# Optimization experiments

Hardware: AMD Instinct MI355X
Metric: run time of the kernel (lower is better)

Reference implementation:

```python
import jax, jax.numpy as jnp
import numpy as np

B, N, M = 4, 8192, 8192


def setup_inputs() -> dict:
    key = jax.random.key(0)
    k1, k2, k3, k4 = jax.random.split(key, 4)
    xyz1 = jax.random.normal(k1, (B, N, 3), dtype=jnp.float32)
    xyz2 = jax.random.normal(k2, (B, M, 3), dtype=jnp.float32)
    weights1 = jax.random.uniform(k3, (B, N), dtype=jnp.float32)
    weights2 = jax.random.uniform(k4, (B, M), dtype=jnp.float32)
    return {"xyz1": xyz1, "xyz2": xyz2, "weights1": weights1, "weights2": weights2}


def _chamfer_dists(xyz1, xyz2):
    # Squared L2 pairwise distances via the ||a||^2 + ||b||^2 - 2 a.b identity
    # (avoids materializing a [B, N, M, 3] difference tensor).
    sq1 = jnp.sum(xyz1 * xyz1, axis=-1)            # [B, N]
    sq2 = jnp.sum(xyz2 * xyz2, axis=-1)            # [B, M]
    dots = jnp.einsum("bnc,bmc->bnm", xyz1, xyz2)  # [B, N, M]
    d = sq1[:, :, None] + sq2[:, None, :] - 2.0 * dots
    d = jnp.maximum(d, 0.0)
    dist1 = jnp.min(d, axis=2)  # [B, N] nearest in xyz2 for each point in xyz1
    dist2 = jnp.min(d, axis=1)  # [B, M] nearest in xyz1 for each point in xyz2
    return dist1, dist2


def reference(xyz1, xyz2, weights1, weights2):
    dist1, dist2 = _chamfer_dists(xyz1, xyz2)
    dist1 = dist1 * weights1
    dist2 = dist2 * weights2
    dist1_avg = jnp.sum(dist1) / jnp.sum(weights1)
    dist2_avg = jnp.sum(dist2) / jnp.sum(weights2)
    return (dist1_avg + dist2_avg) / 2.0
```

## Files before the change

kernel.cpp:

```cpp
#include <hip/hip_runtime.h>

#define TPB 256
constexpr int Bsz  = 4;
constexpr int Npts = 8192;
constexpr int Mpts = 8192;
constexpr int PTS  = Bsz * Npts;
constexpr int Q    = 8;
constexpr int QPB  = TPB * Q;
constexpr int S    = 64;
constexpr int CPS  = Mpts / S;
constexpr int RBLK = 64;

__global__ void __launch_bounds__(TPB, 4) chamfer_min_kernel(
    const float* __restrict__ xyz1, const float* __restrict__ xyz2,
    unsigned int* __restrict__ partials)
{
    const int chunksPerDir = PTS / QPB;
    const int half = chunksPerDir * S;
    int bid = blockIdx.x;
    int dir = (bid >= half) ? 1 : 0;
    int id  = bid - dir * half;
    int s     = id % S;
    int chunk = id / S;
    int batch = chunk / (Npts / QPB);
    int qbase = chunk * QPB + threadIdx.x;

    const float* qsrc = dir ? xyz2 : xyz1;
    const float* csrc = dir ? xyz1 : xyz2;

    __shared__ float4 scand[CPS];
    int c0i = batch * Mpts + s * CPS;
    if (threadIdx.x < CPS) {
        int ci = c0i + threadIdx.x;
        float x = csrc[ci * 3 + 0];
        float y = csrc[ci * 3 + 1];
        float z = csrc[ci * 3 + 2];
        scand[threadIdx.x] =
            make_float4(-2.f * x, -2.f * y, -2.f * z, x * x + y * y + z * z);
    }

    float qx[Q], qy[Q], qz[Q], best[Q];
#pragma unroll
    for (int k = 0; k < Q; ++k) {
        int q = qbase + k * TPB;
        qx[k] = qsrc[q * 3 + 0];
        qy[k] = qsrc[q * 3 + 1];
        qz[k] = qsrc[q * 3 + 2];
        best[k] = 3.4e38f;
    }
    __syncthreads();

#pragma unroll 2
    for (int j = 0; j < CPS; j += 4) {
        float4 c0 = scand[j + 0];
        float4 c1 = scand[j + 1];
        float4 c2 = scand[j + 2];
        float4 c3 = scand[j + 3];
#pragma unroll
        for (int k = 0; k < Q; ++k) {
            float t0 = fmaf(qx[k], c0.x, fmaf(qy[k], c0.y, fmaf(qz[k], c0.z, c0.w)));
            float t1 = fmaf(qx[k], c1.x, fmaf(qy[k], c1.y, fmaf(qz[k], c1.z, c1.w)));
            float t2 = fmaf(qx[k], c2.x, fmaf(qy[k], c2.y, fmaf(qz[k], c2.z, c2.w)));
            float t3 = fmaf(qx[k], c3.x, fmaf(qy[k], c3.y, fmaf(qz[k], c3.z, c3.w)));
            best[k] = fminf(fminf(best[k], t0), t1);
            best[k] = fminf(fminf(best[k], t2), t3);
        }
    }

    unsigned int* pbase = partials + dir * PTS;
#pragma unroll
    for (int k = 0; k < Q; ++k) {
        int q = qbase + k * TPB;
        float sq = fmaf(qx[k], qx[k], fmaf(qy[k], qy[k], qz[k] * qz[k]));
        float d  = fmaxf(best[k] + sq, 0.f);
        atomicMin(&pbase[q], __float_as_uint(d));
    }
}

__global__ void __launch_bounds__(TPB) reduce_kernel(
    const float* __restrict__ partials,
    const float* __restrict__ w1, const float* __restrict__ w2,
    float2* __restrict__ slots)
{
    int gid = blockIdx.x * TPB + threadIdx.x;
    int dir = gid >> 13;
    int idx = gid & 8191;
    const float4* d4 = (const float4*)(partials + (size_t)dir * PTS);
    const float4* w4 = (const float4*)(dir ? w2 : w1);
    float4 d = d4[idx], w = w4[idx];
    float c = d.x * w.x + d.y * w.y + d.z * w.z + d.w * w.w;
    float s = w.x + w.y + w.z + w.w;

    for (int off = 32; off; off >>= 1) {
        c += __shfl_down(c, off);
        s += __shfl_down(s, off);
    }
    __shared__ float sc[4], ss[4];
    int lane = threadIdx.x & 63, wid = threadIdx.x >> 6;
    if (lane == 0) { sc[wid] = c; ss[wid] = s; }
    __syncthreads();
    if (threadIdx.x == 0) {
        slots[blockIdx.x] =
            make_float2(sc[0] + sc[1] + sc[2] + sc[3],
                        ss[0] + ss[1] + ss[2] + ss[3]);
    }
}

__global__ void __launch_bounds__(64) final_kernel(
    const float2* __restrict__ slots, float* __restrict__ out)
{
    float2 v = slots[threadIdx.x];
    for (int off = 16; off; off >>= 1) {
        v.x += __shfl_down(v.x, off, 32);
        v.y += __shfl_down(v.y, off, 32);
    }
    float c1 = __shfl(v.x, 32), s1 = __shfl(v.y, 32);
    if (threadIdx.x == 0)
        out[0] = 0.5f * (v.x / v.y + c1 / s1);
}

extern "C" void kernel_launch(void* const* d_in, const int* in_sizes, int n_in,
                              void* d_out, int out_size, void* d_ws, size_t ws_size,
                              hipStream_t stream) {
    const float* xyz1 = (const float*)d_in[0];
    const float* xyz2 = (const float*)d_in[1];
    const float* w1   = (const float*)d_in[2];
    const float* w2   = (const float*)d_in[3];
    float* out = (float*)d_out;

    unsigned int* partials = (unsigned int*)d_ws;
    float2* slots = (float2*)((char*)d_ws + (size_t)2 * PTS * sizeof(unsigned int));

    int half = (PTS / QPB) * S;
    chamfer_min_kernel<<<2 * half, TPB, 0, stream>>>(xyz1, xyz2, partials);
    reduce_kernel<<<RBLK, TPB, 0, stream>>>((const float*)partials, w1, w2, slots);
    final_kernel<<<1, 64, 0, stream>>>(slots, out);
}
```

Before: 101.0 us.

## Double queries per thread, halve candidate splits, replace atomicMin with per-split partials

```diff
diff --git a/kernel.cpp b/kernel.cpp
--- a/kernel.cpp
+++ b/kernel.cpp
@@ -5,15 +5,15 @@
 constexpr int Npts = 8192;
 constexpr int Mpts = 8192;
 constexpr int PTS  = Bsz * Npts;
-constexpr int Q    = 8;
+constexpr int Q    = 16;
 constexpr int QPB  = TPB * Q;
-constexpr int S    = 64;
+constexpr int S    = 32;
 constexpr int CPS  = Mpts / S;
 constexpr int RBLK = 64;
 
-__global__ void __launch_bounds__(TPB, 4) chamfer_min_kernel(
+__global__ void __launch_bounds__(TPB, 2) chamfer_min_kernel(
     const float* __restrict__ xyz1, const float* __restrict__ xyz2,
-    unsigned int* __restrict__ partials)
+    float* __restrict__ partials)
 {
     const int chunksPerDir = PTS / QPB;
     const int half = chunksPerDir * S;
@@ -29,9 +29,8 @@
     const float* csrc = dir ? xyz1 : xyz2;
 
     __shared__ float4 scand[CPS];
-    int c0i = batch * Mpts + s * CPS;
-    if (threadIdx.x < CPS) {
-        int ci = c0i + threadIdx.x;
+    {
+        int ci = batch * Mpts + s * CPS + threadIdx.x;
         float x = csrc[ci * 3 + 0];
         float y = csrc[ci * 3 + 1];
         float z = csrc[ci * 3 + 2];
@@ -67,13 +66,12 @@
         }
     }
 
-    unsigned int* pbase = partials + dir * PTS;
+    float* pbase = partials + (size_t)s * (2 * PTS) + (size_t)dir * PTS;
 #pragma unroll
     for (int k = 0; k < Q; ++k) {
         int q = qbase + k * TPB;
         float sq = fmaf(qx[k], qx[k], fmaf(qy[k], qy[k], qz[k] * qz[k]));
-        float d  = fmaxf(best[k] + sq, 0.f);
-        atomicMin(&pbase[q], __float_as_uint(d));
+        pbase[q] = fmaxf(best[k] + sq, 0.f);
     }
 }
 
@@ -85,9 +83,16 @@
     int gid = blockIdx.x * TPB + threadIdx.x;
     int dir = gid >> 13;
     int idx = gid & 8191;
-    const float4* d4 = (const float4*)(partials + (size_t)dir * PTS);
-    const float4* w4 = (const float4*)(dir ? w2 : w1);
-    float4 d = d4[idx], w = w4[idx];
+
+    const float4* base = (const float4*)(partials + (size_t)dir * PTS);
+    float4 d = base[idx];
+#pragma unroll 4
+    for (int s = 1; s < S; ++s) {
+        float4 v = base[(size_t)s * (2 * PTS / 4) + idx];
+        d.x = fminf(d.x, v.x); d.y = fminf(d.y, v.y);
+        d.z = fminf(d.z, v.z); d.w = fminf(d.w, v.w);
+    }
+    float4 w = ((const float4*)(dir ? w2 : w1))[idx];
     float c = d.x * w.x + d.y * w.y + d.z * w.z + d.w * w.w;
     float s = w.x + w.y + w.z + w.w;
 
@@ -128,11 +133,11 @@
     const float* w2   = (const float*)d_in[3];
     float* out = (float*)d_out;
 
-    unsigned int* partials = (unsigned int*)d_ws;
-    float2* slots = (float2*)((char*)d_ws + (size_t)2 * PTS * sizeof(unsigned int));
+    float*  partials = (float*)d_ws;
+    float2* slots = (float2*)((char*)d_ws + (size_t)S * 2 * PTS * sizeof(float));
 
     int half = (PTS / QPB) * S;
     chamfer_min_kernel<<<2 * half, TPB, 0, stream>>>(xyz1, xyz2, partials);
-    reduce_kernel<<<RBLK, TPB, 0, stream>>>((const float*)partials, w1, w2, slots);
+    reduce_kernel<<<RBLK, TPB, 0, stream>>>(partials, w1, w2, slots);
     final_kernel<<<1, 64, 0, stream>>>(slots, out);
 }
```

Result: slower. 107.9 us (+6.9%).

## Stream candidates via uniform global loads, drop LDS staging, double queries per thread

Applied to the files above, without the earlier changes.

```diff
diff --git a/kernel.cpp b/kernel.cpp
--- a/kernel.cpp
+++ b/kernel.cpp
@@ -5,13 +5,13 @@
 constexpr int Npts = 8192;
 constexpr int Mpts = 8192;
 constexpr int PTS  = Bsz * Npts;
-constexpr int Q    = 8;
+constexpr int Q    = 16;
 constexpr int QPB  = TPB * Q;
 constexpr int S    = 64;
 constexpr int CPS  = Mpts / S;
 constexpr int RBLK = 64;
 
-__global__ void __launch_bounds__(TPB, 4) chamfer_min_kernel(
+__global__ void __launch_bounds__(TPB) chamfer_min_kernel(
     const float* __restrict__ xyz1, const float* __restrict__ xyz2,
     unsigned int* __restrict__ partials)
 {
@@ -28,40 +28,33 @@
     const float* qsrc = dir ? xyz2 : xyz1;
     const float* csrc = dir ? xyz1 : xyz2;
 
-    __shared__ float4 scand[CPS];
-    int c0i = batch * Mpts + s * CPS;
-    if (threadIdx.x < CPS) {
-        int ci = c0i + threadIdx.x;
-        float x = csrc[ci * 3 + 0];
-        float y = csrc[ci * 3 + 1];
-        float z = csrc[ci * 3 + 2];
-        scand[threadIdx.x] =
-            make_float4(-2.f * x, -2.f * y, -2.f * z, x * x + y * y + z * z);
-    }
-
     float qx[Q], qy[Q], qz[Q], best[Q];
 #pragma unroll
     for (int k = 0; k < Q; ++k) {
         int q = qbase + k * TPB;
-        qx[k] = qsrc[q * 3 + 0];
-        qy[k] = qsrc[q * 3 + 1];
-        qz[k] = qsrc[q * 3 + 2];
+        qx[k] = -2.f * qsrc[q * 3 + 0];
+        qy[k] = -2.f * qsrc[q * 3 + 1];
+        qz[k] = -2.f * qsrc[q * 3 + 2];
         best[k] = 3.4e38f;
     }
-    __syncthreads();
 
+    const float* cp = csrc + (size_t)(batch * Mpts + s * CPS) * 3;
 #pragma unroll 2
     for (int j = 0; j < CPS; j += 4) {
-        float4 c0 = scand[j + 0];
-        float4 c1 = scand[j + 1];
-        float4 c2 = scand[j + 2];
-        float4 c3 = scand[j + 3];
+        float c[12];
+#pragma unroll
+        for (int t = 0; t < 12; ++t)
+            c[t] = cp[j * 3 + t];
+        float w0 = fmaf(c[0], c[0], fmaf(c[1], c[1], c[2]  * c[2]));
+        float w1 = fmaf(c[3], c[3], fmaf(c[4], c[4], c[5]  * c[5]));
+        float w2 = fmaf(c[6], c[6], fmaf(c[7], c[7], c[8]  * c[8]));
+        float w3 = fmaf(c[9], c[9], fmaf(c[10], c[10], c[11] * c[11]));
 #pragma unroll
         for (int k = 0; k < Q; ++k) {
-            float t0 = fmaf(qx[k], c0.x, fmaf(qy[k], c0.y, fmaf(qz[k], c0.z, c0.w)));
-            float t1 = fmaf(qx[k], c1.x, fmaf(qy[k], c1.y, fmaf(qz[k], c1.z, c1.w)));
-            float t2 = fmaf(qx[k], c2.x, fmaf(qy[k], c2.y, fmaf(qz[k], c2.z, c2.w)));
-            float t3 = fmaf(qx[k], c3.x, fmaf(qy[k], c3.y, fmaf(qz[k], c3.z, c3.w)));
+            float t0 = fmaf(qx[k], c[0], fmaf(qy[k], c[1],  fmaf(qz[k], c[2],  w0)));
+            float t1 = fmaf(qx[k], c[3], fmaf(qy[k], c[4],  fmaf(qz[k], c[5],  w1)));
+            float t2 = fmaf(qx[k], c[6], fmaf(qy[k], c[7],  fmaf(qz[k], c[8],  w2)));
+            float t3 = fmaf(qx[k], c[9], fmaf(qy[k], c[10], fmaf(qz[k], c[11], w3)));
             best[k] = fminf(fminf(best[k], t0), t1);
             best[k] = fminf(fminf(best[k], t2), t3);
         }
@@ -71,7 +64,7 @@
 #pragma unroll
     for (int k = 0; k < Q; ++k) {
         int q = qbase + k * TPB;
-        float sq = fmaf(qx[k], qx[k], fmaf(qy[k], qy[k], qz[k] * qz[k]));
+        float sq = 0.25f * fmaf(qx[k], qx[k], fmaf(qy[k], qy[k], qz[k] * qz[k]));
         float d  = fmaxf(best[k] + sq, 0.f);
         atomicMin(&pbase[q], __float_as_uint(d));
     }
```

Measured after the change: 114.0 us. +12.9%, slower.
